# Kernel optimization log

Hardware: AMD Instinct MI355X
Metric: run time of the kernel (lower is better)

## Reference

```python
import jax, jax.numpy as jnp
import numpy as np

OBS_DIM = 32
HIDDEN = 64


def setup_inputs() -> dict:
    key = jax.random.key(0)
    k1, k2, k3, k4 = jax.random.split(key, 4)
    # PyTorch-style uniform init bound 1/sqrt(hidden)
    bnd = 1.0 / np.sqrt(HIDDEN)
    y = jax.random.normal(k1, (256, 2048, OBS_DIM), dtype=jnp.float32)
    Wx = jax.random.uniform(k2, (OBS_DIM, 4 * HIDDEN), minval=-bnd, maxval=bnd, dtype=jnp.float32)
    Wh = jax.random.uniform(k3, (HIDDEN, 4 * HIDDEN), minval=-bnd, maxval=bnd, dtype=jnp.float32)
    b = jax.random.uniform(k4, (4 * HIDDEN,), minval=-bnd, maxval=bnd, dtype=jnp.float32)
    return {"y": y, "Wx": Wx, "Wh": Wh, "b": b}


def reference(y, Wx, Wh, b):
    # y: [B, T, obs_dim] -> LSTM features [B, T, hidden]
    B, T, _ = y.shape
    H = Wh.shape[0]
    yT = jnp.swapaxes(y, 0, 1)  # [T, B, D]

    def step(carry, x_t):
        h, c = carry
        gates = x_t @ Wx + h @ Wh + b  # [B, 4H]
        i, f, g, o = jnp.split(gates, 4, axis=-1)  # PyTorch gate order i,f,g,o
        i = jax.nn.sigmoid(i)
        f = jax.nn.sigmoid(f)
        g = jnp.tanh(g)
        o = jax.nn.sigmoid(o)
        c_new = f * c + i * g
        h_new = o * jnp.tanh(c_new)
        return (h_new, c_new), h_new

    h0 = jnp.zeros((B, H), dtype=y.dtype)
    c0 = jnp.zeros((B, H), dtype=y.dtype)
    _, hs = jax.lax.scan(step, (h0, c0), yT)  # hs: [T, B, H]
    return jnp.swapaxes(hs, 0, 1)  # [B, T, H]
```

## Files before the change

### kernel.cpp

```cpp
#include <hip/hip_runtime.h>

#define BB 256
#define TT 2048
#define DD 32
#define HH 64
#define GG 256
#define OB 8
#define LOG2E 1.44269504088896f

typedef float f32x2 __attribute__((ext_vector_type(2)));
typedef float f32x4 __attribute__((ext_vector_type(4)));

__device__ __forceinline__ float sig_e2(float y) {
    return __builtin_amdgcn_rcpf(1.0f + __builtin_exp2f(-y));
}
__device__ __forceinline__ float rdlane(float v, int k) {
    return __uint_as_float(__builtin_amdgcn_readlane(__float_as_uint(v), k));
}
__device__ __forceinline__ void lds_barrier() {
    asm volatile("s_waitcnt lgkmcnt(0)" ::: "memory");
    __builtin_amdgcn_s_barrier();
    asm volatile("" ::: "memory");
}

__global__ __launch_bounds__(256, 1) void lstm_pk_kernel(
    const float* __restrict__ y,
    const float* __restrict__ Wx,
    const float* __restrict__ Wh,
    const float* __restrict__ b,
    float* __restrict__ out)
{
    const int j = threadIdx.x;
    const int w = j >> 6;
    const int l = j & 63;
    const int batch = blockIdx.x;
    const int kb = 16 * w;

    __shared__ f32x4 gbuf[2][4][HH];
    __shared__ float obuf[2][OB][HH];

    f32x2 whp[4][8];
#pragma unroll
    for (int g = 0; g < 4; ++g)
#pragma unroll
        for (int m = 0; m < 8; ++m) {
            whp[g][m].x = Wh[(kb + 2 * m) * GG + g * HH + l] * LOG2E;
            whp[g][m].y = Wh[(kb + 2 * m + 1) * GG + g * HH + l] * LOG2E;
        }
    float wx[4][8];
#pragma unroll
    for (int g = 0; g < 4; ++g)
#pragma unroll
        for (int d = 0; d < 8; ++d)
            wx[g][d] = Wx[(8 * w + d) * GG + g * HH + l] * LOG2E;
    float bj[4];
#pragma unroll
    for (int g = 0; g < 4; ++g) bj[g] = (w == 0) ? b[g * HH + l] * LOG2E : 0.0f;

    float c = 0.0f, h = 0.0f;

    const float* ybase = y + (size_t)batch * (TT * DD) + 8 * w;
    float* obase = out + (size_t)batch * (TT * HH);

    float4 xa[2], xb[2];
    f32x2 ap[4];
    {
        const float4* r0 = (const float4*)ybase;
        float4 x00 = r0[0], x01 = r0[1];
        const float* xf = (const float*)&x00;
        const float* xg = (const float*)&x01;
#pragma unroll
        for (int g = 0; g < 4; ++g) { ap[g].x = bj[g]; ap[g].y = 0.0f; }
#pragma unroll
        for (int d = 0; d < 4; ++d)
#pragma unroll
            for (int g = 0; g < 4; ++g) ap[g].x = fmaf(xf[d], wx[g][d], ap[g].x);
#pragma unroll
        for (int d = 0; d < 4; ++d)
#pragma unroll
            for (int g = 0; g < 4; ++g) ap[g].y = fmaf(xg[d], wx[g][d + 4], ap[g].y);
        const float4* r1 = (const float4*)(ybase + DD);
        xa[0] = r1[0]; xa[1] = r1[1];
    }
    __syncthreads();

#define STEP(XC, XN, BUFI, TI, TL)                                            \
    {                                                                         \
             \
        _Pragma("unroll")                                                     \
        for (int m = 0; m < 8; ++m) {                                         \
            f32x2 hp;                                                         \
            hp.x = rdlane(h, kb + 2 * m);                                     \
            hp.y = rdlane(h, kb + 2 * m + 1);                                 \
            _Pragma("unroll")                                                 \
            for (int g = 0; g < 4; ++g)                                       \
                ap[g] = __builtin_elementwise_fma(hp, whp[g][m], ap[g]);      \
        }                                                                     \
                   \
        f32x4 pw;                                                             \
        pw.x = ap[0].x + ap[0].y; pw.y = ap[1].x + ap[1].y;                   \
        pw.z = ap[2].x + ap[2].y; pw.w = ap[3].x + ap[3].y;                   \
        gbuf[BUFI][w][l] = pw;                                                \
        \
        {                                                                     \
            const float* xf_ = (const float*)&XC[0];                          \
            _Pragma("unroll")                                                 \
            for (int g = 0; g < 4; ++g) ap[g].x = bj[g];                      \
            _Pragma("unroll")                                                 \
            for (int d = 0; d < 4; ++d)                                       \
                _Pragma("unroll")                                             \
                for (int g = 0; g < 4; ++g)                                   \
                    ap[g].x = fmaf(xf_[d], wx[g][d], ap[g].x);                \
        }                                                                     \
        {                                                                     \
            const int tn_ = ((TI) + 2 < TT) ? ((TI) + 2) : (TT - 1);          \
            const float4* nr_ = (const float4*)(ybase + (size_t)tn_ * DD);    \
            XN[0] = nr_[0]; XN[1] = nr_[1];                                   \
        }                                                                     \
        lds_barrier();                                                        \
                  \
        const f32x4 P0 = gbuf[BUFI][0][l];                                    \
        const f32x4 P1 = gbuf[BUFI][1][l];                                    \
        const f32x4 P2 = gbuf[BUFI][2][l];                                    \
        const f32x4 P3 = gbuf[BUFI][3][l];                                    \
        {                                                                     \
            const float* xg_ = (const float*)&XC[1];                          \
            _Pragma("unroll")                                                 \
            for (int g = 0; g < 4; ++g) ap[g].y = 0.0f;                       \
            _Pragma("unroll")                                                 \
            for (int d = 0; d < 4; ++d)                                       \
                _Pragma("unroll")                                             \
                for (int g = 0; g < 4; ++g)                                   \
                    ap[g].y = fmaf(xg_[d], wx[g][d + 4], ap[g].y);            \
        }                                                                     \
                \
        const f32x4 PS = (P0 + P1) + (P2 + P3);                               \
        const float i_ = sig_e2(PS.x);                                        \
        const float f_ = sig_e2(PS.y);                                        \
        const float g_ = fmaf(2.0f, sig_e2(2.0f * PS.z), -1.0f);    \
        const float o_ = sig_e2(PS.w);                                        \
        c = fmaf(f_, c, i_ * g_);                                             \
        h = o_ * fmaf(2.0f, __builtin_amdgcn_rcpf(                            \
                1.0f + __builtin_exp2f(c * (-2.0f * LOG2E))), -1.0f);         \
        if (w == 0) obuf[obi][TL][l] = h;                                     \
    }

    for (int t0 = 0; t0 < TT; t0 += OB) {
        const int obi = (t0 >> 3) & 1;
#pragma unroll
        for (int tp = 0; tp < OB; tp += 2) {
            STEP(xa, xb, 0, t0 + tp, tp)
            STEP(xb, xa, 1, t0 + tp + 1, tp + 1)
        }
        lds_barrier();
        {
            const int r = j >> 5;
            const int ci = (j & 31) * 2;
            const float2 v = *(const float2*)&obuf[obi][r][ci];
            *(float2*)&obase[(size_t)(t0 + r) * HH + ci] = v;
        }
    }
#undef STEP
}

extern "C" void kernel_launch(void* const* d_in, const int* in_sizes, int n_in,
                              void* d_out, int out_size, void* d_ws, size_t ws_size,
                              hipStream_t stream) {
    const float* y  = (const float*)d_in[0];
    const float* Wx = (const float*)d_in[1];
    const float* Wh = (const float*)d_in[2];
    const float* b  = (const float*)d_in[3];
    float* out = (float*)d_out;

    lstm_pk_kernel<<<BB, GG, 0, stream>>>(y, Wx, Wh, b, out);
}
```

Measured before the change: 1.069 ms.

## Split recurrent K-reduction across eight waves instead of four

Launches 512 threads per batch block so each of eight waves handles 8 hidden inputs and 4 observation dims, down from 16 and 8. This halves the serial readlane/FMA chain per step on the critical recurrent path, and drops the packed f32x2 math in favour of scalar FMAs over two accumulators. In exchange each step now reads and sums eight partial gate vectors from LDS, and the barrier must synchronise eight waves. The output store becomes one float per thread.

Measured after the change: 1.225 ms. 1.15x slower.

```diff
diff --git a/kernel.cpp b/kernel.cpp
--- a/kernel.cpp
+++ b/kernel.cpp
@@ -8,7 +8,6 @@
 #define OB 8
 #define LOG2E 1.44269504088896f
 
-typedef float f32x2 __attribute__((ext_vector_type(2)));
 typedef float f32x4 __attribute__((ext_vector_type(4)));
 
 __device__ __forceinline__ float sig_e2(float y) {
@@ -23,99 +22,83 @@
     asm volatile("" ::: "memory");
 }
 
-__global__ __launch_bounds__(256, 1) void lstm_pk_kernel(
+__global__ __launch_bounds__(512, 1) void lstm_k8_kernel(
     const float* __restrict__ y,
     const float* __restrict__ Wx,
     const float* __restrict__ Wh,
     const float* __restrict__ b,
     float* __restrict__ out)
 {
-    const int j = threadIdx.x;
-    const int w = j >> 6;
-    const int l = j & 63;
+    const int tid = threadIdx.x;
+    const int wv  = tid >> 6;
+    const int l   = tid & 63;
     const int batch = blockIdx.x;
-    const int kb = 16 * w;
+    const int kb  = 8 * wv;
 
-    __shared__ f32x4 gbuf[2][4][HH];
+    __shared__ f32x4 gbuf[2][8][HH];
     __shared__ float obuf[2][OB][HH];
 
-    f32x2 whp[4][8];
+    float wh[4][8];
 #pragma unroll
     for (int g = 0; g < 4; ++g)
 #pragma unroll
-        for (int m = 0; m < 8; ++m) {
-            whp[g][m].x = Wh[(kb + 2 * m) * GG + g * HH + l] * LOG2E;
-            whp[g][m].y = Wh[(kb + 2 * m + 1) * GG + g * HH + l] * LOG2E;
-        }
-    float wx[4][8];
+        for (int k = 0; k < 8; ++k)
+            wh[g][k] = Wh[(kb + k) * GG + g * HH + l] * LOG2E;
+    float wx4[4][4];
 #pragma unroll
     for (int g = 0; g < 4; ++g)
 #pragma unroll
-        for (int d = 0; d < 8; ++d)
-            wx[g][d] = Wx[(8 * w + d) * GG + g * HH + l] * LOG2E;
+        for (int d = 0; d < 4; ++d)
+            wx4[g][d] = Wx[(4 * wv + d) * GG + g * HH + l] * LOG2E;
     float bj[4];
 #pragma unroll
-    for (int g = 0; g < 4; ++g) bj[g] = (w == 0) ? b[g * HH + l] * LOG2E : 0.0f;
+    for (int g = 0; g < 4; ++g) bj[g] = (wv == 0) ? b[g * HH + l] * LOG2E : 0.0f;
 
     float c = 0.0f, h = 0.0f;
 
-    const float* ybase = y + (size_t)batch * (TT * DD) + 8 * w;
+    const float* ybase = y + (size_t)batch * (TT * DD) + 4 * wv;
     float* obase = out + (size_t)batch * (TT * HH);
 
-    float4 xa[2], xb[2];
-    f32x2 ap[4];
+    float4 xa, xb;
+    float a0[4], a1[4];
     {
-        const float4* r0 = (const float4*)ybase;
-        float4 x00 = r0[0], x01 = r0[1];
-        const float* xf = (const float*)&x00;
-        const float* xg = (const float*)&x01;
+        const float4 x0 = *(const float4*)ybase;
 #pragma unroll
-        for (int g = 0; g < 4; ++g) { ap[g].x = bj[g]; ap[g].y = 0.0f; }
-#pragma unroll
-        for (int d = 0; d < 4; ++d)
-#pragma unroll
-            for (int g = 0; g < 4; ++g) ap[g].x = fmaf(xf[d], wx[g][d], ap[g].x);
-#pragma unroll
-        for (int d = 0; d < 4; ++d)
-#pragma unroll
-            for (int g = 0; g < 4; ++g) ap[g].y = fmaf(xg[d], wx[g][d + 4], ap[g].y);
-        const float4* r1 = (const float4*)(ybase + DD);
-        xa[0] = r1[0]; xa[1] = r1[1];
+        for (int g = 0; g < 4; ++g) {
+            a0[g] = fmaf(x0.y, wx4[g][1], fmaf(x0.x, wx4[g][0], bj[g]));
+            a1[g] = fmaf(x0.w, wx4[g][3], x0.z * wx4[g][2]);
+        }
+        xa = *(const float4*)(ybase + DD);
     }
     __syncthreads();
 
 #define STEP(XC, XN, BUFI, TI, TL)                                            \
     {                                                                         \
-             \
+                    \
         _Pragma("unroll")                                                     \
-        for (int m = 0; m < 8; ++m) {                                         \
-            f32x2 hp;                                                         \
-            hp.x = rdlane(h, kb + 2 * m);                                     \
-            hp.y = rdlane(h, kb + 2 * m + 1);                                 \
+        for (int k = 0; k < 4; ++k) {                                         \
+            const float hk = rdlane(h, kb + k);                               \
             _Pragma("unroll")                                                 \
-            for (int g = 0; g < 4; ++g)                                       \
-                ap[g] = __builtin_elementwise_fma(hp, whp[g][m], ap[g]);      \
+            for (int g = 0; g < 4; ++g) a0[g] = fmaf(hk, wh[g][k], a0[g]);    \
         }                                                                     \
-                   \
+        _Pragma("unroll")                                                     \
+        for (int k = 4; k < 8; ++k) {                                         \
+            const float hk = rdlane(h, kb + k);                               \
+            _Pragma("unroll")                                                 \
+            for (int g = 0; g < 4; ++g) a1[g] = fmaf(hk, wh[g][k], a1[g]);    \
+        }                                                                     \
+                          \
         f32x4 pw;                                                             \
-        pw.x = ap[0].x + ap[0].y; pw.y = ap[1].x + ap[1].y;                   \
-        pw.z = ap[2].x + ap[2].y; pw.w = ap[3].x + ap[3].y;                   \
-        gbuf[BUFI][w][l] = pw;                                                \
+        pw.x = a0[0] + a1[0]; pw.y = a0[1] + a1[1];                           \
+        pw.z = a0[2] + a1[2]; pw.w = a0[3] + a1[3];                           \
+        gbuf[BUFI][wv][l] = pw;                                               \
         \
-        {                                                                     \
-            const float* xf_ = (const float*)&XC[0];                          \
-            _Pragma("unroll")                                                 \
-            for (int g = 0; g < 4; ++g) ap[g].x = bj[g];                      \
-            _Pragma("unroll")                                                 \
-            for (int d = 0; d < 4; ++d)                                       \
-                _Pragma("unroll")                                             \
-                for (int g = 0; g < 4; ++g)                                   \
-                    ap[g].x = fmaf(xf_[d], wx[g][d], ap[g].x);                \
-        }                                                                     \
+        _Pragma("unroll")                                                     \
+        for (int g = 0; g < 4; ++g)                                           \
+            a0[g] = fmaf(XC.y, wx4[g][1], fmaf(XC.x, wx4[g][0], bj[g]));      \
         {                                                                     \
             const int tn_ = ((TI) + 2 < TT) ? ((TI) + 2) : (TT - 1);          \
-            const float4* nr_ = (const float4*)(ybase + (size_t)tn_ * DD);    \
-            XN[0] = nr_[0]; XN[1] = nr_[1];                                   \
+            XN = *(const float4*)(ybase + (size_t)tn_ * DD);                  \
         }                                                                     \
         lds_barrier();                                                        \
                   \
@@ -123,18 +106,15 @@
         const f32x4 P1 = gbuf[BUFI][1][l];                                    \
         const f32x4 P2 = gbuf[BUFI][2][l];                                    \
         const f32x4 P3 = gbuf[BUFI][3][l];                                    \
-        {                                                                     \
-            const float* xg_ = (const float*)&XC[1];                          \
-            _Pragma("unroll")                                                 \
-            for (int g = 0; g < 4; ++g) ap[g].y = 0.0f;                       \
-            _Pragma("unroll")                                                 \
-            for (int d = 0; d < 4; ++d)                                       \
-                _Pragma("unroll")                                             \
-                for (int g = 0; g < 4; ++g)                                   \
-                    ap[g].y = fmaf(xg_[d], wx[g][d + 4], ap[g].y);            \
-        }                                                                     \
-                \
-        const f32x4 PS = (P0 + P1) + (P2 + P3);                               \
+        const f32x4 P4 = gbuf[BUFI][4][l];                                    \
+        const f32x4 P5 = gbuf[BUFI][5][l];                                    \
+        const f32x4 P6 = gbuf[BUFI][6][l];                                    \
+        const f32x4 P7 = gbuf[BUFI][7][l];                                    \
+        _Pragma("unroll")                                                     \
+        for (int g = 0; g < 4; ++g)                                           \
+            a1[g] = fmaf(XC.w, wx4[g][3], XC.z * wx4[g][2]);                  \
+         \
+        const f32x4 PS = ((P0 + P1) + (P2 + P3)) + ((P4 + P5) + (P6 + P7));   \
         const float i_ = sig_e2(PS.x);                                        \
         const float f_ = sig_e2(PS.y);                                        \
         const float g_ = fmaf(2.0f, sig_e2(2.0f * PS.z), -1.0f);    \
@@ -142,7 +122,7 @@
         c = fmaf(f_, c, i_ * g_);                                             \
         h = o_ * fmaf(2.0f, __builtin_amdgcn_rcpf(                            \
                 1.0f + __builtin_exp2f(c * (-2.0f * LOG2E))), -1.0f);         \
-        if (w == 0) obuf[obi][TL][l] = h;                                     \
+        if (wv == 0) obuf[obi][TL][l] = h;                                    \
     }
 
     for (int t0 = 0; t0 < TT; t0 += OB) {
@@ -154,10 +134,9 @@
         }
         lds_barrier();
         {
-            const int r = j >> 5;
-            const int ci = (j & 31) * 2;
-            const float2 v = *(const float2*)&obuf[obi][r][ci];
-            *(float2*)&obase[(size_t)(t0 + r) * HH + ci] = v;
+            const int r  = tid >> 6;
+            const int ci = tid & 63;
+            obase[(size_t)(t0 + r) * HH + ci] = obuf[obi][r][ci];
         }
     }
 #undef STEP
@@ -172,5 +151,5 @@
     const float* b  = (const float*)d_in[3];
     float* out = (float*)d_out;
 
-    lstm_pk_kernel<<<BB, GG, 0, stream>>>(y, Wx, Wh, b, out);
+    lstm_k8_kernel<<<BB, 512, 0, stream>>>(y, Wx, Wh, b, out);
 }
```
